# Performance work log

Hardware: AMD Instinct MI355X
Metric: run time of the kernel (lower is better)

Reference implementation:

```python
import math
import jax, jax.numpy as jnp
import numpy as np

EMBED_DIM = 1024
NUM_HEADS = 16
HEAD_DIM = EMBED_DIM // NUM_HEADS


def setup_inputs() -> dict:
    key = jax.random.key(0)
    k1, k2, k3, k4 = jax.random.split(key, 4)
    B, S = 4, 2048
    x = jax.random.normal(k1, (B, S, EMBED_DIM), dtype=jnp.float32)
    mask = jnp.ones((B, S), dtype=jnp.int32)  # key-padding mask, 1 = keep
    # nn.Linear(embed_dim, 3*embed_dim, bias=False): weight [3E, E]
    w_qkv = jax.random.normal(k2, (3 * EMBED_DIM, EMBED_DIM), dtype=jnp.float32) / math.sqrt(EMBED_DIM)
    # nn.Linear(embed_dim, embed_dim): weight [E, E], bias [E]
    w_out = jax.random.normal(k3, (EMBED_DIM, EMBED_DIM), dtype=jnp.float32) / math.sqrt(EMBED_DIM)
    b_out = jax.random.normal(k4, (EMBED_DIM,), dtype=jnp.float32) * 0.01
    return {"x": x, "w_qkv": w_qkv, "w_out": w_out, "b_out": b_out, "mask": mask}


def _attention(x, w_qkv, w_out, b_out, mask):
    B, S, E = x.shape
    qkv = jnp.einsum("bse,fe->bsf", x, w_qkv)  # [B,S,3E]
    q, k, v = jnp.split(qkv, 3, axis=-1)
    def heads(t):  # [B,S,E] -> [B,H,S,D]
        return t.reshape(B, S, NUM_HEADS, HEAD_DIM).transpose(0, 2, 1, 3)
    q, k, v = heads(q), heads(k), heads(v)
    scores = jnp.einsum("bhqd,bhkd->bhqk", q, k) / math.sqrt(HEAD_DIM)
    keep = (mask != 0)[:, None, None, :]  # [B,1,1,S]
    scores = jnp.where(keep, scores, jnp.float32(-1e9))
    probs = jax.nn.softmax(scores, axis=-1)
    # dropout p=0.0 -> identity (eval semantics)
    out = jnp.einsum("bhqk,bhkd->bhqd", probs, v)
    out = out.transpose(0, 2, 1, 3).reshape(B, S, E)
    return jnp.einsum("bse,fe->bsf", out, w_out) + b_out


def reference(x, w_qkv, w_out, b_out, mask):
    return _attention(x, w_qkv, w_out, b_out, mask)
```

## Files before the change

### kernel.cpp

```cpp
#include <hip/hip_runtime.h>

#define EMB 1024
#define NH 16
#define HD 64
#define SEQ 2048
#define BB 4

typedef __attribute__((ext_vector_type(8))) short bf8;
typedef __attribute__((ext_vector_type(4))) short bf4;
typedef __attribute__((ext_vector_type(4))) float f4;

#define MFMA16(a, b, c) __builtin_amdgcn_mfma_f32_16x16x32_bf16((a), (b), (c), 0, 0, 0)

#if defined(__has_builtin)
#if __has_builtin(__builtin_amdgcn_mfma_f32_16x16x16_bf16_1k)
#define HAVE_MFMA16X16 1
#endif
#if __has_builtin(__builtin_amdgcn_exp2f)
#define EXP2F __builtin_amdgcn_exp2f
#endif
#if __has_builtin(__builtin_amdgcn_cvt_pk_bf16_f32)
#define HAVE_PK_BF16 1
#endif
#if __has_builtin(__builtin_amdgcn_perm)
#define HAVE_PERM 1
#endif
#endif
#ifndef EXP2F
#define EXP2F exp2f
#endif

__device__ inline f4 pv_mfma(bf4 a, bf4 b, f4 c) {
#ifdef HAVE_MFMA16X16
  return __builtin_amdgcn_mfma_f32_16x16x16_bf16_1k(a, b, c, 0, 0, 0);
#else
  bf8 av, bv;
  *(bf4*)&av = a;  ((int*)&av)[2] = 0; ((int*)&av)[3] = 0;
  *(bf4*)&bv = b;  ((int*)&bv)[2] = 0; ((int*)&bv)[3] = 0;
  return __builtin_amdgcn_mfma_f32_16x16x32_bf16(av, bv, c, 0, 0, 0);
#endif
}

#define GLL16(g, l)                                                     \
  __builtin_amdgcn_global_load_lds(                                     \
      (__attribute__((address_space(1))) void*)(g),                     \
      (__attribute__((address_space(3))) void*)(l), 16, 0, 0)

__device__ inline unsigned short f2bf(float f) {
  union { float f; unsigned u; } v; v.f = f;
  unsigned u = v.u;
  u += 0x7fffu + ((u >> 16) & 1u);
  return (unsigned short)(u >> 16);
}

__device__ inline unsigned pkbf(float a, float b) {
#ifdef HAVE_PK_BF16
  typedef __attribute__((ext_vector_type(2))) __bf16 bf16x2;
  union { bf16x2 v; unsigned u; } c;
  c.v = __builtin_amdgcn_cvt_pk_bf16_f32(a, b);
  return c.u;
#elif defined(HAVE_PERM)
  union { float f; unsigned u; } ua, ub; ua.f = a; ub.f = b;
  return __builtin_amdgcn_perm(ub.u + 0x8000u, ua.u + 0x8000u, 0x07060302u);
#else
  union { float f; unsigned u; } ua, ub; ua.f = a; ub.f = b;
  return ((ua.u + 0x8000u) >> 16) | ((ub.u + 0x8000u) & 0xFFFF0000u);
#endif
}

#define SCALE_LOG2E 0.1803368801111244f

__global__ void cvt_all(const float* __restrict__ x, const float* __restrict__ wq,
                        const float* __restrict__ wo, unsigned short* __restrict__ out) {
  int i = blockIdx.x * blockDim.x + threadIdx.x;
  float4 f;
  if (i < 2097152)      f = ((const float4*)x)[i];
  else if (i < 2883584) f = ((const float4*)wq)[i - 2097152];
  else                  f = ((const float4*)wo)[i - 2883584];
  ushort4 o;
  o.x = f2bf(f.x); o.y = f2bf(f.y); o.z = f2bf(f.z); o.w = f2bf(f.w);
  ((ushort4*)out)[i] = o;
}

template <bool OUTF32>
__global__ __launch_bounds__(256, 2) void gemm_bt(
    const unsigned short* __restrict__ A, const unsigned short* __restrict__ B,
    void* __restrict__ Cout, const float* __restrict__ bias,
    unsigned short* __restrict__ vtb,
    int M, int N, int K, int ldC, int nsplit) {
  __shared__ unsigned short la[128 * 32];
  __shared__ unsigned short lb[128 * 32];

  const int t = threadIdx.x;
  const int lane = t & 63;
  const int w = t >> 6;
  const int quad = lane >> 4;
  const int lcol = lane & 15;

  const int nbx = gridDim.x;
  const int flat = blockIdx.y * nbx + blockIdx.x;
  const int nper = (nbx * gridDim.y) >> 3;
  const int sw = (flat & 7) * nper + (flat >> 3);
  const int m0 = (sw / nbx) * 128;
  const int n0 = (sw % nbx) * 128;

  const int wm = (w & 1) * 64;
  const int wn = (w >> 1) * 64;

  f4 acc[4][4];
#pragma unroll
  for (int i = 0; i < 4; i++)
#pragma unroll
    for (int j = 0; j < 4; j++) acc[i][j] = (f4){0.f, 0.f, 0.f, 0.f};

  const int srow = t >> 2;
  const int scol = (t & 3) * 8;
  const unsigned short* gA = A + (size_t)(m0 + srow) * K + scol;
  const unsigned short* gB = B + (size_t)(n0 + srow) * K + scol;
  unsigned short* lA = la + t * 8;
  unsigned short* lB = lb + t * 8;

  for (int kt = 0; kt < K; kt += 32) {
    __syncthreads();
    GLL16(gA + kt, lA);
    GLL16(gA + kt + (size_t)64 * K, lA + 64 * 32);
    GLL16(gB + kt, lB);
    GLL16(gB + kt + (size_t)64 * K, lB + 64 * 32);
    __syncthreads();

    bf8 af[4], bfr[4];
#pragma unroll
    for (int i = 0; i < 4; i++) {
      af[i]  = *(const bf8*)&la[(wm + i * 16 + lcol) * 32 + quad * 8];
      bfr[i] = *(const bf8*)&lb[(wn + i * 16 + lcol) * 32 + quad * 8];
    }
#pragma unroll
    for (int i = 0; i < 4; i++)
#pragma unroll
      for (int j = 0; j < 4; j++)
        acc[i][j] = MFMA16(af[i], bfr[j], acc[i][j]);
  }

  if (!OUTF32 && n0 >= nsplit) {
#pragma unroll
    for (int i = 0; i < 4; i++) {
#pragma unroll
      for (int j = 0; j < 4; j++) {
        int f = n0 + wn + j * 16 + lcol - nsplit;
        int mg = m0 + wm + i * 16 + quad * 4;
        int bb = mg >> 11, ss = mg & 2047;
        ushort4 pk;
        pk.x = f2bf(acc[i][j][0]); pk.y = f2bf(acc[i][j][1]);
        pk.z = f2bf(acc[i][j][2]); pk.w = f2bf(acc[i][j][3]);
        *(ushort4*)&vtb[((size_t)(bb * 1024 + f)) * 2048 + ss] = pk;
      }
    }
  } else {
#pragma unroll
    for (int i = 0; i < 4; i++) {
#pragma unroll
      for (int j = 0; j < 4; j++) {
        int n = n0 + wn + j * 16 + lcol;
        const float scl = (!OUTF32 && n >= 1024) ? SCALE_LOG2E : 1.f;
#pragma unroll
        for (int r = 0; r < 4; r++) {
          int m = m0 + wm + i * 16 + quad * 4 + r;
          if (OUTF32) {
            float v = acc[i][j][r] + (bias ? bias[n] : 0.f);
            ((float*)Cout)[(size_t)m * ldC + n] = v;
          } else {
            ((unsigned short*)Cout)[(size_t)m * ldC + n] = f2bf(acc[i][j][r] * scl);
          }
        }
      }
    }
  }
}

#define BKEEP (-16.0f)
#define BDROP (-1e30f)

__global__ __launch_bounds__(512, 4) void attn_kernel(
    const unsigned short* __restrict__ qk, const unsigned short* __restrict__ vtg,
    const int* __restrict__ mask, unsigned short* __restrict__ outb) {
  __shared__ unsigned short kv[2 * 16384];
  __shared__ __align__(16) float bt[2][128];

  const int t = threadIdx.x;
  const int lane = t & 63;
  const int w = t >> 6;
  const int quad = lane >> 4;
  const int lcol = lane & 15;
  const int lx = lcol & 7;

  const int id = blockIdx.x + (blockIdx.y << 4) + (blockIdx.z << 8);
  const int g  = (id & 7) + ((id >> 7) << 3);
  const int q0 = ((id >> 3) & 15) * 128;
  const int h = g & 15;
  const int b = g >> 4;

  const unsigned short* qbase = qk + (size_t)(b * SEQ) * 2048 + h * HD;
  const unsigned short* kbase = qbase + 1024;
  const unsigned short* vbase = vtg + (size_t)((b * 16 + h) * 64) * SEQ;

  const int qrow = q0 + w * 16 + lcol;
  const bf8 qf0 = *(const bf8*)(qbase + (size_t)qrow * 2048 + quad * 8);
  const bf8 qf1 = *(const bf8*)(qbase + (size_t)qrow * 2048 + 32 + quad * 8);

  f4 o[4];
#pragma unroll
  for (int db = 0; db < 4; db++) o[db] = (f4){0.f, 0.f, 0.f, 0.f};
  float lsum = 0.f;

  const int sr = t >> 3;
  const int sc = ((t & 7) ^ (sr & 7)) * 8;
  const unsigned short* gk = kbase + (size_t)sr * 2048 + sc;
  const int vd = t >> 4;
  const int vc8 = ((t & 15) ^ (vd & 7)) * 8;
  const unsigned short* gv = vbase + (size_t)vd * SEQ + vc8;

  const int NT = SEQ / 128;

  GLL16(gk, kv + t * 8);
  GLL16(gk + (size_t)64 * 2048, kv + 4096 + t * 8);
  GLL16(gv, kv + 8192 + t * 8);
  GLL16(gv + (size_t)32 * SEQ, kv + 12288 + t * 8);
  if (t < 128) bt[0][t] = mask[b * SEQ + t] ? BKEEP : BDROP;
  int pmv = (t < 128) ? mask[b * SEQ + 128 + t] : 0;

  for (int it = 0; it < NT; ++it) {
    const int cur = (it & 1) * 16384;
    __syncthreads();

    if (it + 1 < NT) {
      const int nxt = ((it + 1) & 1) * 16384;
      const size_t k1 = (size_t)(it + 1) * 128;
      GLL16(gk + k1 * 2048, kv + nxt + t * 8);
      GLL16(gk + (k1 + 64) * 2048, kv + nxt + 4096 + t * 8);
      GLL16(gv + k1, kv + nxt + 8192 + t * 8);
      GLL16(gv + (size_t)32 * SEQ + k1, kv + nxt + 12288 + t * 8);
      if (t < 128) bt[(it + 1) & 1][t] = pmv ? BKEEP : BDROP;
      int kn = (it + 2 < NT) ? (it + 2) * 128 : 0;
      pmv = (t < 128) ? mask[b * SEQ + kn + t] : 0;
    }

    const unsigned short* kcur = kv + cur;
    const unsigned short* vcur = kv + cur + 8192;
    const float* bcur = bt[it & 1];

#pragma unroll
    for (int hh = 0; hh < 2; hh++) {
      f4 sT[4];
      __builtin_amdgcn_s_setprio(1);
#pragma unroll
      for (int kb = 0; kb < 4; kb++) {
        const unsigned short* krow = kcur + (hh * 64 + kb * 16 + lcol) * 64;
        bf8 kf0 = *(const bf8*)&krow[(quad ^ lx) * 8];
        bf8 kf1 = *(const bf8*)&krow[((4 + quad) ^ lx) * 8];
        f4 a = *(const f4*)&bcur[hh * 64 + kb * 16 + quad * 4];
        a = MFMA16(kf0, qf0, a);
        a = MFMA16(kf1, qf1, a);
        sT[kb] = a;
      }
      __builtin_amdgcn_s_setprio(0);

      bf4 pfrag[4];
#pragma unroll
      for (int kb = 0; kb < 4; kb++) {
        float p0 = EXP2F(sT[kb][0]);
        float p1 = EXP2F(sT[kb][1]);
        float p2 = EXP2F(sT[kb][2]);
        float p3 = EXP2F(sT[kb][3]);
        lsum += (p0 + p1) + (p2 + p3);
        union { unsigned u[2]; bf4 s; } cv;
        cv.u[0] = pkbf(p0, p1);
        cv.u[1] = pkbf(p2, p3);
        pfrag[kb] = cv.s;
      }

      __builtin_amdgcn_s_setprio(1);
#pragma unroll
      for (int db = 0; db < 4; db++) {
        const unsigned short* vrow = vcur + (db * 16 + lcol) * 128;
#pragma unroll
        for (int kb = 0; kb < 4; kb++) {
          int c = ((hh * 4 + kb) << 1) | (quad >> 1);
          bf4 vf = *(const bf4*)&vrow[(c ^ lx) * 8 + (quad & 1) * 4];
          o[db] = pv_mfma(vf, pfrag[kb], o[db]);
        }
      }
      __builtin_amdgcn_s_setprio(0);
    }
  }

  lsum += __shfl_xor(lsum, 16);
  lsum += __shfl_xor(lsum, 32);
  float inv = 1.f / lsum;
#pragma unroll
  for (int db = 0; db < 4; db++) {
    ushort4 pk;
    pk.x = f2bf(o[db][0] * inv);
    pk.y = f2bf(o[db][1] * inv);
    pk.z = f2bf(o[db][2] * inv);
    pk.w = f2bf(o[db][3] * inv);
    *(ushort4*)&outb[(size_t)(b * SEQ + q0 + w * 16 + lcol) * EMB + h * HD +
                     db * 16 + quad * 4] = pk;
  }
}

extern "C" void kernel_launch(void* const* d_in, const int* in_sizes, int n_in,
                              void* d_out, int out_size, void* d_ws, size_t ws_size,
                              hipStream_t stream) {
  const float* x     = (const float*)d_in[0];
  const float* w_qkv = (const float*)d_in[1];
  const float* w_out = (const float*)d_in[2];
  const float* b_out = (const float*)d_in[3];
  const int*   mask  = (const int*)d_in[4];

  char* ws = (char*)d_ws;
  unsigned short* xb    = (unsigned short*)(ws + 0);
  unsigned short* wqkvb = (unsigned short*)(ws + 16777216);
  unsigned short* woutb = (unsigned short*)(ws + 23068672);
  unsigned short* qkb   = (unsigned short*)(ws + 25165824);
  unsigned short* attnb = (unsigned short*)(ws + 58720256);
  unsigned short* vtb   = (unsigned short*)(ws + 75497472);

  cvt_all<<<12288, 256, 0, stream>>>(x, w_qkv, w_out, (unsigned short*)ws);

  gemm_bt<false><<<dim3(24, 64), 256, 0, stream>>>(
      xb, wqkvb, (void*)qkb, nullptr, vtb, 8192, 3072, 1024, 2048, 2048);

  attn_kernel<<<dim3(16, 16, 4), 512, 0, stream>>>(qkb, vtb, mask, attnb);

  gemm_bt<true><<<dim3(8, 64), 256, 0, stream>>>(
      attnb, woutb, d_out, b_out, nullptr, 8192, 1024, 1024, 1024, 1 << 30);
}
```

Baseline: 306.4 us.

## Double-buffer LDS tiles in the bf16 GEMM to prefetch the next K-slice

The GEMM now keeps two LDS buffers for the A and B tiles. It issues the global-to-LDS loads for the next 32-wide K-slice before computing MFMAs on the current one, which removes one barrier per iteration and hides load latency behind compute. The launch-bounds occupancy hint also goes from 2 to 3 blocks per CU, even though LDS use per block doubles. This may push register allocation tighter. Correctness relies on the barrier at the top of each iteration waiting for the outstanding async loads.

```diff
diff --git a/kernel.cpp b/kernel.cpp
--- a/kernel.cpp
+++ b/kernel.cpp
@@ -83,13 +83,13 @@
 }
 
 template <bool OUTF32>
-__global__ __launch_bounds__(256, 2) void gemm_bt(
+__global__ __launch_bounds__(256, 3) void gemm_bt(
     const unsigned short* __restrict__ A, const unsigned short* __restrict__ B,
     void* __restrict__ Cout, const float* __restrict__ bias,
     unsigned short* __restrict__ vtb,
     int M, int N, int K, int ldC, int nsplit) {
-  __shared__ unsigned short la[128 * 32];
-  __shared__ unsigned short lb[128 * 32];
+  __shared__ unsigned short la[2][128 * 32];
+  __shared__ unsigned short lb[2][128 * 32];
 
   const int t = threadIdx.x;
   const int lane = t & 63;
@@ -117,22 +117,31 @@
   const int scol = (t & 3) * 8;
   const unsigned short* gA = A + (size_t)(m0 + srow) * K + scol;
   const unsigned short* gB = B + (size_t)(n0 + srow) * K + scol;
-  unsigned short* lA = la + t * 8;
-  unsigned short* lB = lb + t * 8;
-
-  for (int kt = 0; kt < K; kt += 32) {
+
+  GLL16(gA, la[0] + t * 8);
+  GLL16(gA + (size_t)64 * K, la[0] + 64 * 32 + t * 8);
+  GLL16(gB, lb[0] + t * 8);
+  GLL16(gB + (size_t)64 * K, lb[0] + 64 * 32 + t * 8);
+
+  const int nk = K >> 5;
+  for (int it = 0; it < nk; ++it) {
+    const int cur = it & 1;
     __syncthreads();
-    GLL16(gA + kt, lA);
-    GLL16(gA + kt + (size_t)64 * K, lA + 64 * 32);
-    GLL16(gB + kt, lB);
-    GLL16(gB + kt + (size_t)64 * K, lB + 64 * 32);
-    __syncthreads();
+
+    if (it + 1 < nk) {
+      const int nxt = cur ^ 1;
+      const int kt = (it + 1) << 5;
+      GLL16(gA + kt, la[nxt] + t * 8);
+      GLL16(gA + kt + (size_t)64 * K, la[nxt] + 64 * 32 + t * 8);
+      GLL16(gB + kt, lb[nxt] + t * 8);
+      GLL16(gB + kt + (size_t)64 * K, lb[nxt] + 64 * 32 + t * 8);
+    }
 
     bf8 af[4], bfr[4];
 #pragma unroll
     for (int i = 0; i < 4; i++) {
-      af[i]  = *(const bf8*)&la[(wm + i * 16 + lcol) * 32 + quad * 8];
-      bfr[i] = *(const bf8*)&lb[(wn + i * 16 + lcol) * 32 + quad * 8];
+      af[i]  = *(const bf8*)&la[cur][(wm + i * 16 + lcol) * 32 + quad * 8];
+      bfr[i] = *(const bf8*)&lb[cur][(wn + i * 16 + lcol) * 32 + quad * 8];
     }
 #pragma unroll
     for (int i = 0; i < 4; i++)
```

Result: no change. 305.8 us (median of 2 runs) (-0.2%).
